# Optimization experiments

Hardware: AMD Instinct MI355X
Metric: run time of the kernel (lower is better)

The kernel has to match this reference:

```python
import jax, jax.numpy as jnp
import numpy as np


def setup_inputs() -> dict:
    key = jax.random.key(0)
    k1, k2, k3, k4, k5 = jax.random.split(key, 5)
    B, Ci, Co, H, W, N, K = 8, 256, 256, 128, 128, 4, 3
    x = jax.random.normal(k1, (B, Ci, H, W), dtype=jnp.float32)
    weight = jax.random.normal(k2, (N, Co, Ci, K, K), dtype=jnp.float32)
    styles = jax.random.normal(k3, (B, Ci), dtype=jnp.float32)
    selector = jax.random.uniform(k4, (B, N), dtype=jnp.float32)
    noise = jax.random.normal(k5, (B, Co, H, W), dtype=jnp.float32)
    return {"x": x, "weight": weight, "styles": styles,
            "selector": selector, "noise": noise}


def reference(x, weight, styles, selector, noise):
    """Modulated conv2d with adaptive kernel selection (fused_modconv path).

    x:        [B, Ci, H, W]
    weight:   [N, Co, Ci, kh, kw]  kernel bank
    styles:   [B, Ci]              modulation
    selector: [B, N]               adaptive kernel mixing coefficients
    noise:    [B, Co, H, W]        additive noise
    """
    B, Ci, H, W = x.shape
    N, Co, _, kh, kw = weight.shape

    # adaptive kernel selection: per-sample kernel = selector-weighted sum of bank
    w = jnp.einsum('bn,noihw->boihw', selector, weight)          # [B,Co,Ci,kh,kw]

    # modulate by styles
    w = w * styles[:, None, :, None, None]

    # demodulate
    dcoefs = jax.lax.rsqrt(jnp.sum(w * w, axis=(2, 3, 4)) + 1e-8)  # [B,Co]
    w = w * dcoefs[:, :, None, None, None]

    # fused per-sample conv via grouped conv (groups = B), cross-correlation
    # (flip_weight=True in the torch code means plain conv2d / cross-correlation)
    xr = x.reshape(1, B * Ci, H, W)
    wr = w.reshape(B * Co, Ci, kh, kw)
    out = jax.lax.conv_general_dilated(
        xr, wr,
        window_strides=(1, 1),
        padding=[(kh // 2, kh // 2), (kw // 2, kw // 2)],
        feature_group_count=B,
        dimension_numbers=('NCHW', 'OIHW', 'NCHW'),
    )
    out = out.reshape(B, Co, H, W) + noise
    return out
```

## Files before the change

### kernel.cpp

```cpp
#include <hip/hip_runtime.h>


typedef __attribute__((ext_vector_type(4))) float f32x4;
typedef __attribute__((ext_vector_type(8))) short s16x8;

#define NB   8
#define NCI  256
#define NCO  256
#define NHW  128
#define NKER 4

#define SB0 __builtin_amdgcn_sched_barrier(0)
#define BAR __builtin_amdgcn_s_barrier()
#define WAITL0 asm volatile("s_waitcnt lgkmcnt(0)" ::: "memory")

__device__ __forceinline__ unsigned short f2bf(float f) {
  unsigned int u = __builtin_bit_cast(unsigned int, f);
  u += 0x7FFFu + ((u >> 16) & 1u);
  return (unsigned short)(u >> 16);
}

__global__ __launch_bounds__(256) void prep_k(
    const float* __restrict__ weight,
    const float* __restrict__ styles,
    const float* __restrict__ selector,
    unsigned short* __restrict__ wmod)
{
  int bid = blockIdx.x;
  int b = bid >> 8, co = bid & 255;
  int ci = threadIdx.x;

  float sel[NKER];
#pragma unroll
  for (int n = 0; n < NKER; ++n) sel[n] = selector[b * NKER + n];

  float a[9];
#pragma unroll
  for (int j = 0; j < 9; ++j) a[j] = 0.f;
#pragma unroll
  for (int n = 0; n < NKER; ++n) {
    const float* wp = weight + (size_t)((n * NCO + co) * NCI + ci) * 9;
    float s = sel[n];
#pragma unroll
    for (int j = 0; j < 9; ++j) a[j] += s * wp[j];
  }
  float st = styles[b * NCI + ci];
  float ss = 0.f;
#pragma unroll
  for (int j = 0; j < 9; ++j) { a[j] *= st; ss += a[j] * a[j]; }

  for (int off = 32; off; off >>= 1) ss += __shfl_down(ss, off, 64);
  __shared__ float red[4];
  int wid = threadIdx.x >> 6, lane = threadIdx.x & 63;
  if (lane == 0) red[wid] = ss;
  __syncthreads();
  float tot = red[0] + red[1] + red[2] + red[3];
  float d = rsqrtf(tot + 1e-8f);

  int kb = ci >> 5;
  size_t base = (size_t)(co >> 4) * 512 +
                (size_t)(((ci & 31) >> 3) * 128) + ((co & 15) * 8) + (ci & 7);
#pragma unroll
  for (int j = 0; j < 9; ++j) {
    size_t T = (size_t)((b * 9 + j) * 8 + kb);
    wmod[(T << 13) + base] = f2bf(a[j] * d);
  }
}

__global__ __launch_bounds__(256, 2) void conv_k(
    const float* __restrict__ x,
    const unsigned short* __restrict__ wg,
    const float* __restrict__ noise,
    float* __restrict__ out)
{
  extern __shared__ __align__(16) char XRs[];

  int orig = blockIdx.x;
  int b = orig & 7;
  int h = orig >> 3;

  int t = threadIdx.x;
  int lane = t & 63;
  int wid = t >> 6;
  int cow = wid << 6;
  int ll = lane & 15;
  int ks = lane >> 4;

  f32x4 acc[4][8];
#pragma unroll
  for (int m = 0; m < 4; ++m)
#pragma unroll
    for (int n = 0; n < 8; ++n) acc[m][n] = (f32x4){0.f, 0.f, 0.f, 0.f};

  int c = ((t >> 4) & 15) * 2;
  int wi = t & 15;
  float xlo[8], xhi[8];
  unsigned xmask = 0xFFFFFFFFu;

  auto issueX = [&](int g) {
    int gc = g < 24 ? g : 23;
    int dh = gc >> 3, kb = gc & 7;
    int hy = h + dh - 1;
    xmask = ((unsigned)hy < 128u) ? 0xFFFFFFFFu : 0u;
    int hyc = hy < 0 ? 0 : (hy > 127 ? 127 : hy);
    const float* base = x + ((size_t)(b * NCI + kb * 32 + c) * NHW + hyc) * NHW + wi;
#pragma unroll
    for (int j2 = 0; j2 < 8; ++j2) {
      xlo[j2] = base[j2 * 16];
      xhi[j2] = base[NHW * NHW + j2 * 16];
    }
  };

  auto issueAF = [&](int tc, s16x8* af) {
    if (tc > 71) tc = 71;
    int g = tc / 3, tap = tc - g * 3;
    int dh = g >> 3, kb = g & 7;
    const char* src = (const char*)wg +
        ((size_t)((b * 9 + dh * 3 + tap) * 8 + kb) << 14) + wid * 4096 + lane * 16;
#pragma unroll
    for (int m = 0; m < 4; ++m)
      af[m] = *(const s16x8*)(src + m * 1024);
  };

  auto packXR = [&](int g) {
    char* dstb = XRs + (g & 1) * 8192;
    int slot = (((wi & 1) << 2) + (c >> 3)) ^ ((wi >> 1) & 7);
    char* p0 = dstb + (wi >> 1) * 128 + (slot << 4) + ((c & 7) << 1);
#pragma unroll
    for (int j2 = 0; j2 < 8; ++j2) {
      unsigned pk = ((unsigned)f2bf(xhi[j2]) << 16) | f2bf(xlo[j2]);
      *(unsigned*)(p0 + j2 * 1024) = pk & xmask;
    }
  };

#define PFB(XRBASE, DW, bf)                                              \
  {                                                                      \
    const char* Xb = (XRBASE);                                           \
    _Pragma("unroll")                                                    \
    for (int n = 0; n < 8; ++n) {                                        \
      int wn = n * 16 + ll + (DW) - 1;                                   \
      if (((DW) == 0 && n == 0) || ((DW) == 2 && n == 7)) {              \
        int wx = wn < 0 ? 0 : (wn > 127 ? 127 : wn);                     \
        int row = wx >> 1;                                               \
        int slot = (((wx & 1) << 2) + ks) ^ (row & 7);                   \
        s16x8 bv = *(const s16x8*)(Xb + row * 128 + (slot << 4));        \
        if (wn != wx) { s16x8 z = {0, 0, 0, 0, 0, 0, 0, 0}; bv = z; }    \
        bf[n] = bv;                                                      \
      } else {                                                           \
        int row = wn >> 1;                                               \
        int slot = (((wn & 1) << 2) + ks) ^ (row & 7);                   \
        bf[n] = *(const s16x8*)(Xb + row * 128 + (slot << 4));           \
      }                                                                  \
    }                                                                    \
  }

#define MFMA32(af, bf)                                                   \
  __builtin_amdgcn_s_setprio(1);                                         \
  _Pragma("unroll")                                                      \
  for (int m = 0; m < 4; ++m)                                            \
    _Pragma("unroll")                                                    \
    for (int n = 0; n < 8; ++n)                                          \
      acc[m][n] = __builtin_amdgcn_mfma_f32_16x16x32_bf16(               \
          af[m], bf[n], acc[m][n], 0, 0, 0);                             \
  __builtin_amdgcn_s_setprio(0);

  s16x8 afA[4], afB[4], bf[8];

  issueX(0); SB0;
  issueAF(0, afA); SB0;
  packXR(0);

#pragma unroll 1
  for (int gg = 0; gg < 12; ++gg) {
    int g0 = gg * 2, t0 = gg * 6;
    WAITL0; SB0; BAR; SB0;
    PFB(XRs, 0, bf);
    issueAF(t0 + 1, afB); SB0;
    issueX(g0 + 1); SB0;
    MFMA32(afA, bf);
    PFB(XRs, 1, bf);
    issueAF(t0 + 2, afA); SB0;
    MFMA32(afB, bf);
    PFB(XRs, 2, bf);
    issueAF(t0 + 3, afB); SB0;
    packXR(g0 + 1);
    MFMA32(afA, bf);
    WAITL0; SB0; BAR; SB0;
    PFB(XRs + 8192, 0, bf);
    issueAF(t0 + 4, afA); SB0;
    issueX(g0 + 2); SB0;
    MFMA32(afB, bf);
    PFB(XRs + 8192, 1, bf);
    issueAF(t0 + 5, afB); SB0;
    MFMA32(afA, bf);
    PFB(XRs + 8192, 2, bf);
    issueAF(t0 + 6, afA); SB0;
    packXR(g0 + 2);
    MFMA32(afB, bf);
  }

  int pr4 = ks * 4;
#pragma unroll
  for (int m = 0; m < 4; ++m) {
#pragma unroll
    for (int n = 0; n < 8; ++n) {
      int px = n * 16 + ll;
#pragma unroll
      for (int j = 0; j < 4; ++j) {
        int co = cow + m * 16 + pr4 + j;
        size_t idx = ((size_t)(b * NCO + co) * NHW + h) * NHW + px;
        out[idx] = acc[m][n][j] + noise[idx];
      }
    }
  }
}

extern "C" void kernel_launch(void* const* d_in, const int* in_sizes, int n_in,
                              void* d_out, int out_size, void* d_ws, size_t ws_size,
                              hipStream_t stream) {
  const float* x        = (const float*)d_in[0];
  const float* weight   = (const float*)d_in[1];
  const float* styles   = (const float*)d_in[2];
  const float* selector = (const float*)d_in[3];
  const float* noise    = (const float*)d_in[4];
  float* out = (float*)d_out;

  unsigned short* wmod = (unsigned short*)d_ws;

  hipLaunchKernelGGL(prep_k, dim3(NB * NCO), dim3(256), 0, stream,
                     weight, styles, selector, wmod);
  hipLaunchKernelGGL(conv_k, dim3(NB * NHW), dim3(256), 16 * 1024, stream,
                     x, wmod, noise, out);
}
```

Baseline: 174.5 us.

## Pad LDS X tile with zero halo columns and precompute B-fragment offsets

Shifts the shared-memory X tile by one pixel pair and adds zeroed halo rows on both sides, so the width-boundary clamp/zero logic in the B-fragment loads goes away and each load is a base offset plus an immediate. Precomputes the per-lane swizzled offsets for the three horizontal taps. It also swaps the rounded bf16 conversion in the pack step for a cheaper add-and-byte-permute, and replaces the row mask with a branch. The LDS footprint grows slightly, and the bf16 rounding changes from round-to-nearest-even to round-half-up.

```diff
diff --git a/kernel.cpp b/kernel.cpp
--- a/kernel.cpp
+++ b/kernel.cpp
@@ -9,6 +9,7 @@
 #define NCO  256
 #define NHW  128
 #define NKER 4
+#define XRS  8448
 
 #define SB0 __builtin_amdgcn_sched_barrier(0)
 #define BAR __builtin_amdgcn_s_barrier()
@@ -92,16 +93,28 @@
 #pragma unroll
     for (int n = 0; n < 8; ++n) acc[m][n] = (f32x4){0.f, 0.f, 0.f, 0.f};
 
+  int bofs[3];
+#pragma unroll
+  for (int dw = 0; dw < 3; ++dw) {
+    int w0 = ll + dw + 1;
+    int row0 = w0 >> 1;
+    int slot0 = (((w0 & 1) << 2) + ks) ^ (row0 & 7);
+    bofs[dw] = row0 * 128 + slot0 * 16;
+  }
+
   int c = ((t >> 4) & 15) * 2;
   int wi = t & 15;
+  int prow = (wi + 2) >> 1;
+  int pslot = (((wi & 1) << 2) + (c >> 3)) ^ (prow & 7);
+  int pbase = prow * 128 + pslot * 16 + ((c & 7) << 1);
   float xlo[8], xhi[8];
-  unsigned xmask = 0xFFFFFFFFu;
+  int hvalid = 1;
 
   auto issueX = [&](int g) {
     int gc = g < 24 ? g : 23;
     int dh = gc >> 3, kb = gc & 7;
     int hy = h + dh - 1;
-    xmask = ((unsigned)hy < 128u) ? 0xFFFFFFFFu : 0u;
+    hvalid = ((unsigned)hy < 128u);
     int hyc = hy < 0 ? 0 : (hy > 127 ? 127 : hy);
     const float* base = x + ((size_t)(b * NCI + kb * 32 + c) * NHW + hyc) * NHW + wi;
 #pragma unroll
@@ -123,35 +136,27 @@
   };
 
   auto packXR = [&](int g) {
-    char* dstb = XRs + (g & 1) * 8192;
-    int slot = (((wi & 1) << 2) + (c >> 3)) ^ ((wi >> 1) & 7);
-    char* p0 = dstb + (wi >> 1) * 128 + (slot << 4) + ((c & 7) << 1);
-#pragma unroll
-    for (int j2 = 0; j2 < 8; ++j2) {
-      unsigned pk = ((unsigned)f2bf(xhi[j2]) << 16) | f2bf(xlo[j2]);
-      *(unsigned*)(p0 + j2 * 1024) = pk & xmask;
+    char* p0 = XRs + (g & 1) * XRS + pbase;
+    if (hvalid) {
+#pragma unroll
+      for (int j2 = 0; j2 < 8; ++j2) {
+        unsigned uhi = __builtin_bit_cast(unsigned, xhi[j2]) + 0x8000u;
+        unsigned ulo = __builtin_bit_cast(unsigned, xlo[j2]) + 0x8000u;
+        *(unsigned*)(p0 + j2 * 1024) = __builtin_amdgcn_perm(uhi, ulo, 0x07060302u);
+      }
+    } else {
+#pragma unroll
+      for (int j2 = 0; j2 < 8; ++j2)
+        *(unsigned*)(p0 + j2 * 1024) = 0u;
     }
   };
 
-#define PFB(XRBASE, DW, bf)                                              \
+#define PFB(BUFIMM, DW, bf)                                              \
   {                                                                      \
-    const char* Xb = (XRBASE);                                           \
+    const char* Xb = XRs + bofs[DW] + (BUFIMM);                          \
     _Pragma("unroll")                                                    \
-    for (int n = 0; n < 8; ++n) {                                        \
-      int wn = n * 16 + ll + (DW) - 1;                                   \
-      if (((DW) == 0 && n == 0) || ((DW) == 2 && n == 7)) {              \
-        int wx = wn < 0 ? 0 : (wn > 127 ? 127 : wn);                     \
-        int row = wx >> 1;                                               \
-        int slot = (((wx & 1) << 2) + ks) ^ (row & 7);                   \
-        s16x8 bv = *(const s16x8*)(Xb + row * 128 + (slot << 4));        \
-        if (wn != wx) { s16x8 z = {0, 0, 0, 0, 0, 0, 0, 0}; bv = z; }    \
-        bf[n] = bv;                                                      \
-      } else {                                                           \
-        int row = wn >> 1;                                               \
-        int slot = (((wn & 1) << 2) + ks) ^ (row & 7);                   \
-        bf[n] = *(const s16x8*)(Xb + row * 128 + (slot << 4));           \
-      }                                                                  \
-    }                                                                    \
+    for (int n = 0; n < 8; ++n)                                          \
+      bf[n] = *(const s16x8*)(Xb + n * 1024);                            \
   }
 
 #define MFMA32(af, bf)                                                   \
@@ -166,6 +171,11 @@
 
   s16x8 afA[4], afB[4], bf[8];
 
+  if (t < 32) {
+    int rg = t >> 3;
+    char* gz = XRs + (rg >> 1) * XRS + ((rg & 1) ? 65 * 128 : 0) + (t & 7) * 16;
+    *(f32x4*)gz = (f32x4){0.f, 0.f, 0.f, 0.f};
+  }
   issueX(0); SB0;
   issueAF(0, afA); SB0;
   packXR(0);
@@ -174,26 +184,26 @@
   for (int gg = 0; gg < 12; ++gg) {
     int g0 = gg * 2, t0 = gg * 6;
     WAITL0; SB0; BAR; SB0;
-    PFB(XRs, 0, bf);
+    PFB(0, 0, bf);
     issueAF(t0 + 1, afB); SB0;
     issueX(g0 + 1); SB0;
     MFMA32(afA, bf);
-    PFB(XRs, 1, bf);
+    PFB(0, 1, bf);
     issueAF(t0 + 2, afA); SB0;
     MFMA32(afB, bf);
-    PFB(XRs, 2, bf);
+    PFB(0, 2, bf);
     issueAF(t0 + 3, afB); SB0;
     packXR(g0 + 1);
     MFMA32(afA, bf);
     WAITL0; SB0; BAR; SB0;
-    PFB(XRs + 8192, 0, bf);
+    PFB(XRS, 0, bf);
     issueAF(t0 + 4, afA); SB0;
     issueX(g0 + 2); SB0;
     MFMA32(afB, bf);
-    PFB(XRs + 8192, 1, bf);
+    PFB(XRS, 1, bf);
     issueAF(t0 + 5, afB); SB0;
     MFMA32(afA, bf);
-    PFB(XRs + 8192, 2, bf);
+    PFB(XRS, 2, bf);
     issueAF(t0 + 6, afA); SB0;
     packXR(g0 + 2);
     MFMA32(afB, bf);
@@ -229,6 +239,6 @@
 
   hipLaunchKernelGGL(prep_k, dim3(NB * NCO), dim3(256), 0, stream,
                      weight, styles, selector, wmod);
-  hipLaunchKernelGGL(conv_k, dim3(NB * NHW), dim3(256), 16 * 1024, stream,
+  hipLaunchKernelGGL(conv_k, dim3(NB * NHW), dim3(256), 2 * XRS, stream,
                      x, wmod, noise, out);
 }
```

New measurement: 194.3 us. +11.3%, slower.

## Split conv output channels across two blocks and use 2x2 wave tiling

Applied to the files above, without the earlier changes.

The conv kernel grid is doubled so each block computes 128 output channels instead of 256, and the four waves are arranged as a 2x2 grid over channels and pixel columns. This halves the accumulator registers per wave, allowing three blocks per CU via launch bounds. The pipeline is also reworked with double B-fragment buffers and explicit vmcnt waits. In exchange, each block loads and packs the same input row twice (once per channel half), so x traffic and conversion work double.

```diff
diff --git a/kernel.cpp b/kernel.cpp
--- a/kernel.cpp
+++ b/kernel.cpp
@@ -12,7 +12,8 @@
 
 #define SB0 __builtin_amdgcn_sched_barrier(0)
 #define BAR __builtin_amdgcn_s_barrier()
-#define WAITL0 asm volatile("s_waitcnt lgkmcnt(0)" ::: "memory")
+#define WAITV(N) asm volatile("s_waitcnt vmcnt(" #N ")" ::: "memory")
+#define WAITL0   asm volatile("s_waitcnt lgkmcnt(0)" ::: "memory")
 
 __device__ __forceinline__ unsigned short f2bf(float f) {
   unsigned int u = __builtin_bit_cast(unsigned int, f);
@@ -67,7 +68,7 @@
   }
 }
 
-__global__ __launch_bounds__(256, 2) void conv_k(
+__global__ __launch_bounds__(256, 3) void conv_k(
     const float* __restrict__ x,
     const unsigned short* __restrict__ wg,
     const float* __restrict__ noise,
@@ -77,20 +78,22 @@
 
   int orig = blockIdx.x;
   int b = orig & 7;
-  int h = orig >> 3;
+  int rem = orig >> 3;
+  int h = rem >> 1;
+  int cot = rem & 1;
 
   int t = threadIdx.x;
   int lane = t & 63;
   int wid = t >> 6;
-  int cow = wid << 6;
+  int wr = wid >> 1, wc = wid & 1;
   int ll = lane & 15;
   int ks = lane >> 4;
 
-  f32x4 acc[4][8];
+  f32x4 acc[4][4];
 #pragma unroll
   for (int m = 0; m < 4; ++m)
 #pragma unroll
-    for (int n = 0; n < 8; ++n) acc[m][n] = (f32x4){0.f, 0.f, 0.f, 0.f};
+    for (int n = 0; n < 4; ++n) acc[m][n] = (f32x4){0.f, 0.f, 0.f, 0.f};
 
   int c = ((t >> 4) & 15) * 2;
   int wi = t & 15;
@@ -116,7 +119,8 @@
     int g = tc / 3, tap = tc - g * 3;
     int dh = g >> 3, kb = g & 7;
     const char* src = (const char*)wg +
-        ((size_t)((b * 9 + dh * 3 + tap) * 8 + kb) << 14) + wid * 4096 + lane * 16;
+        ((size_t)((b * 9 + dh * 3 + tap) * 8 + kb) << 14) +
+        cot * 8192 + wr * 4096 + lane * 16;
 #pragma unroll
     for (int m = 0; m < 4; ++m)
       af[m] = *(const s16x8*)(src + m * 1024);
@@ -137,9 +141,9 @@
   {                                                                      \
     const char* Xb = (XRBASE);                                           \
     _Pragma("unroll")                                                    \
-    for (int n = 0; n < 8; ++n) {                                        \
-      int wn = n * 16 + ll + (DW) - 1;                                   \
-      if (((DW) == 0 && n == 0) || ((DW) == 2 && n == 7)) {              \
+    for (int n = 0; n < 4; ++n) {                                        \
+      int wn = wc * 64 + n * 16 + ll + (DW) - 1;                         \
+      if (((DW) == 0 && n == 0) || ((DW) == 2 && n == 3)) {              \
         int wx = wn < 0 ? 0 : (wn > 127 ? 127 : wn);                     \
         int row = wx >> 1;                                               \
         int slot = (((wx & 1) << 2) + ks) ^ (row & 7);                   \
@@ -154,60 +158,67 @@
     }                                                                    \
   }
 
-#define MFMA32(af, bf)                                                   \
+#define MFMA16(af, bf)                                                   \
   __builtin_amdgcn_s_setprio(1);                                         \
   _Pragma("unroll")                                                      \
   for (int m = 0; m < 4; ++m)                                            \
     _Pragma("unroll")                                                    \
-    for (int n = 0; n < 8; ++n)                                          \
+    for (int n = 0; n < 4; ++n)                                          \
       acc[m][n] = __builtin_amdgcn_mfma_f32_16x16x32_bf16(               \
           af[m], bf[n], acc[m][n], 0, 0, 0);                             \
   __builtin_amdgcn_s_setprio(0);
 
-  s16x8 afA[4], afB[4], bf[8];
+  s16x8 afA[4], afB[4], bf0[4], bf1[4];
 
   issueX(0); SB0;
-  issueAF(0, afA); SB0;
+  issueAF(0, afB); SB0;
+  WAITV(4); SB0;
   packXR(0);
 
 #pragma unroll 1
   for (int gg = 0; gg < 12; ++gg) {
     int g0 = gg * 2, t0 = gg * 6;
     WAITL0; SB0; BAR; SB0;
-    PFB(XRs, 0, bf);
-    issueAF(t0 + 1, afB); SB0;
+    PFB(XRs, 0, bf0);
+    PFB(XRs, 1, bf1);
+    issueAF(t0 + 1, afA); SB0;
     issueX(g0 + 1); SB0;
-    MFMA32(afA, bf);
-    PFB(XRs, 1, bf);
-    issueAF(t0 + 2, afA); SB0;
-    MFMA32(afB, bf);
-    PFB(XRs, 2, bf);
-    issueAF(t0 + 3, afB); SB0;
+    WAITV(20); SB0;
+    MFMA16(afB, bf0);
+    issueAF(t0 + 2, afB); SB0;
+    PFB(XRs, 2, bf0);
+    WAITV(20); SB0;
+    MFMA16(afA, bf1);
+    issueAF(t0 + 3, afA); SB0;
+    WAITV(4); SB0;
     packXR(g0 + 1);
-    MFMA32(afA, bf);
+    MFMA16(afB, bf0);
     WAITL0; SB0; BAR; SB0;
-    PFB(XRs + 8192, 0, bf);
-    issueAF(t0 + 4, afA); SB0;
+    PFB(XRs + 8192, 0, bf0);
+    PFB(XRs + 8192, 1, bf1);
+    issueAF(t0 + 4, afB); SB0;
     issueX(g0 + 2); SB0;
-    MFMA32(afB, bf);
-    PFB(XRs + 8192, 1, bf);
-    issueAF(t0 + 5, afB); SB0;
-    MFMA32(afA, bf);
-    PFB(XRs + 8192, 2, bf);
-    issueAF(t0 + 6, afA); SB0;
+    WAITV(20); SB0;
+    MFMA16(afA, bf0);
+    issueAF(t0 + 5, afA); SB0;
+    PFB(XRs + 8192, 2, bf0);
+    WAITV(20); SB0;
+    MFMA16(afB, bf1);
+    issueAF(t0 + 6, afB); SB0;
+    WAITV(4); SB0;
     packXR(g0 + 2);
-    MFMA32(afB, bf);
+    MFMA16(afA, bf0);
   }
 
   int pr4 = ks * 4;
 #pragma unroll
   for (int m = 0; m < 4; ++m) {
 #pragma unroll
-    for (int n = 0; n < 8; ++n) {
-      int px = n * 16 + ll;
+    for (int n = 0; n < 4; ++n) {
+      int px = wc * 64 + n * 16 + ll;
 #pragma unroll
       for (int j = 0; j < 4; ++j) {
-        int co = cow + m * 16 + pr4 + j;
+        int co = cot * 128 + wr * 64 + m * 16 + pr4 + j;
         size_t idx = ((size_t)(b * NCO + co) * NHW + h) * NHW + px;
         out[idx] = acc[m][n][j] + noise[idx];
       }
@@ -229,6 +240,6 @@
 
   hipLaunchKernelGGL(prep_k, dim3(NB * NCO), dim3(256), 0, stream,
                      weight, styles, selector, wmod);
-  hipLaunchKernelGGL(conv_k, dim3(NB * NHW), dim3(256), 16 * 1024, stream,
+  hipLaunchKernelGGL(conv_k, dim3(NB * 2 * NHW), dim3(256), 16 * 1024, stream,
                      x, wmod, noise, out);
 }
```

Result: slower. 209.4 us (+20.0%).

## Interleave next-tap LDS B-fragment reads with MFMAs and use zero pad slot

Applied to the files above, without the earlier changes.

Reorders the inner MFMA loop so that each B-fragment column's LDS read for the next kernel tap is issued alongside the four MFMAs for the current column, pinned in place with sched_group_barrier. This hides LDS latency behind matrix work instead of doing a full fragment prefetch between MFMA blocks. Edge columns outside the image now read from a small zeroed LDS region rather than being clamped and then masked with a select. The change adds 256 bytes of LDS and keeps more live registers, which could affect occupancy at two blocks per CU.

```diff
diff --git a/kernel.cpp b/kernel.cpp
--- a/kernel.cpp
+++ b/kernel.cpp
@@ -13,6 +13,7 @@
 #define SB0 __builtin_amdgcn_sched_barrier(0)
 #define BAR __builtin_amdgcn_s_barrier()
 #define WAITL0 asm volatile("s_waitcnt lgkmcnt(0)" ::: "memory")
+#define ZOFF 16384
 
 __device__ __forceinline__ unsigned short f2bf(float f) {
   unsigned int u = __builtin_bit_cast(unsigned int, f);
@@ -133,39 +134,54 @@
     }
   };
 
-#define PFB(XRBASE, DW, bf)                                              \
+#define RDB(BUFOFF, DW, n, dst)                                          \
   {                                                                      \
-    const char* Xb = (XRBASE);                                           \
+    int wn = (n) * 16 + ll + (DW) - 1;                                   \
+    int row = wn >> 1;                                                   \
+    int slot = (((wn & 1) << 2) + ks) ^ (row & 7);                       \
+    int a = (BUFOFF) + row * 128 + (slot << 4);                          \
+    if (((DW) == 0 && (n) == 0) || ((DW) == 2 && (n) == 7)) {            \
+      if ((unsigned)wn > 127u) a = ZOFF + (ks << 4);                     \
+    }                                                                    \
+    dst = *(const s16x8*)(XRs + a);                                      \
+  }
+
+#define PFB0(BUFOFF, DW, bf)                                             \
+  {                                                                      \
     _Pragma("unroll")                                                    \
-    for (int n = 0; n < 8; ++n) {                                        \
-      int wn = n * 16 + ll + (DW) - 1;                                   \
-      if (((DW) == 0 && n == 0) || ((DW) == 2 && n == 7)) {              \
-        int wx = wn < 0 ? 0 : (wn > 127 ? 127 : wn);                     \
-        int row = wx >> 1;                                               \
-        int slot = (((wx & 1) << 2) + ks) ^ (row & 7);                   \
-        s16x8 bv = *(const s16x8*)(Xb + row * 128 + (slot << 4));        \
-        if (wn != wx) { s16x8 z = {0, 0, 0, 0, 0, 0, 0, 0}; bv = z; }    \
-        bf[n] = bv;                                                      \
-      } else {                                                           \
-        int row = wn >> 1;                                               \
-        int slot = (((wn & 1) << 2) + ks) ^ (row & 7);                   \
-        bf[n] = *(const s16x8*)(Xb + row * 128 + (slot << 4));           \
-      }                                                                  \
-    }                                                                    \
-  }
-
-#define MFMA32(af, bf)                                                   \
+    for (int n = 0; n < 8; ++n) RDB(BUFOFF, DW, n, bf[n]);               \
+  }
+
+#define TILE_ILV(AF, DWN, BUFOFF)                                        \
   __builtin_amdgcn_s_setprio(1);                                         \
   _Pragma("unroll")                                                      \
-  for (int m = 0; m < 4; ++m)                                            \
+  for (int n = 0; n < 8; ++n) {                                          \
+    s16x8 tnew;                                                          \
+    RDB(BUFOFF, DWN, n, tnew);                                           \
+    __builtin_amdgcn_sched_group_barrier(0x100, 1, 0);                   \
     _Pragma("unroll")                                                    \
-    for (int n = 0; n < 8; ++n)                                          \
+    for (int m = 0; m < 4; ++m)                                          \
       acc[m][n] = __builtin_amdgcn_mfma_f32_16x16x32_bf16(               \
-          af[m], bf[n], acc[m][n], 0, 0, 0);                             \
+          AF[m], bfc[n], acc[m][n], 0, 0, 0);                            \
+    __builtin_amdgcn_sched_group_barrier(0x008, 4, 0);                   \
+    bfc[n] = tnew;                                                       \
+  }                                                                      \
   __builtin_amdgcn_s_setprio(0);
 
-  s16x8 afA[4], afB[4], bf[8];
-
+#define TILE_LAST(AF)                                                    \
+  __builtin_amdgcn_s_setprio(1);                                         \
+  _Pragma("unroll")                                                      \
+  for (int n = 0; n < 8; ++n)                                            \
+    _Pragma("unroll")                                                    \
+    for (int m = 0; m < 4; ++m)                                          \
+      acc[m][n] = __builtin_amdgcn_mfma_f32_16x16x32_bf16(               \
+          AF[m], bfc[n], acc[m][n], 0, 0, 0);                            \
+  __builtin_amdgcn_s_setprio(0);
+
+  s16x8 afA[4], afB[4], bfc[8];
+
+  if (t < 16)
+    *(f32x4*)(XRs + ZOFF + t * 16) = (f32x4){0.f, 0.f, 0.f, 0.f};
   issueX(0); SB0;
   issueAF(0, afA); SB0;
   packXR(0);
@@ -174,29 +190,25 @@
   for (int gg = 0; gg < 12; ++gg) {
     int g0 = gg * 2, t0 = gg * 6;
     WAITL0; SB0; BAR; SB0;
-    PFB(XRs, 0, bf);
+    PFB0(0, 0, bfc);
     issueAF(t0 + 1, afB); SB0;
     issueX(g0 + 1); SB0;
-    MFMA32(afA, bf);
-    PFB(XRs, 1, bf);
+    TILE_ILV(afA, 1, 0);
     issueAF(t0 + 2, afA); SB0;
-    MFMA32(afB, bf);
-    PFB(XRs, 2, bf);
+    TILE_ILV(afB, 2, 0);
     issueAF(t0 + 3, afB); SB0;
     packXR(g0 + 1);
-    MFMA32(afA, bf);
+    TILE_LAST(afA);
     WAITL0; SB0; BAR; SB0;
-    PFB(XRs + 8192, 0, bf);
+    PFB0(8192, 0, bfc);
     issueAF(t0 + 4, afA); SB0;
     issueX(g0 + 2); SB0;
-    MFMA32(afB, bf);
-    PFB(XRs + 8192, 1, bf);
+    TILE_ILV(afB, 1, 8192);
     issueAF(t0 + 5, afB); SB0;
-    MFMA32(afA, bf);
-    PFB(XRs + 8192, 2, bf);
+    TILE_ILV(afA, 2, 8192);
     issueAF(t0 + 6, afA); SB0;
     packXR(g0 + 2);
-    MFMA32(afB, bf);
+    TILE_LAST(afB);
   }
 
   int pr4 = ks * 4;
@@ -229,6 +241,6 @@
 
   hipLaunchKernelGGL(prep_k, dim3(NB * NCO), dim3(256), 0, stream,
                      weight, styles, selector, wmod);
-  hipLaunchKernelGGL(conv_k, dim3(NB * NHW), dim3(256), 16 * 1024, stream,
+  hipLaunchKernelGGL(conv_k, dim3(NB * NHW), dim3(256), 16640, stream,
                      x, wmod, noise, out);
 }
```

New measurement: 174.4 us. No clear change (-0.0%).
